# Kernel optimization log

Hardware: AMD Instinct MI355X
Metric: run time of the kernel (lower is better)

## Reference

```python
import jax, jax.numpy as jnp
import numpy as np

D_MODEL = 1024
H = 16
D_K = D_MODEL // H
MAX_SEQ_LEN = 2048
B = 2
S = 2048


def setup_inputs() -> dict:
    key = jax.random.key(0)
    ks = jax.random.split(key, 8)
    scale = 1.0 / np.sqrt(D_MODEL)
    return {
        "q": jax.random.normal(ks[0], (B, S, D_MODEL), jnp.float32),
        "k": jax.random.normal(ks[1], (B, S, D_MODEL), jnp.float32),
        "v": jax.random.normal(ks[2], (B, S, D_MODEL), jnp.float32),
        "mask": jnp.ones((B, 1, S, S), dtype=bool),
        "w_q": jax.random.normal(ks[3], (D_MODEL, D_MODEL), jnp.float32) * scale,
        "w_k": jax.random.normal(ks[4], (D_MODEL, D_MODEL), jnp.float32) * scale,
        "w_v": jax.random.normal(ks[5], (D_MODEL, D_MODEL), jnp.float32) * scale,
        "w_o": jax.random.normal(ks[6], (D_MODEL, D_MODEL), jnp.float32) * scale,
        "rel_emb": jax.random.normal(ks[7], (2 * MAX_SEQ_LEN - 1, H), jnp.float32) * 0.02,
    }


def reference(q, k, v, mask, w_q, w_k, w_v, w_o, rel_emb):
    batch, seq_len, _ = q.shape
    # projections (nn.Linear without bias: x @ W.T)
    query = (q @ w_q.T).reshape(batch, seq_len, H, D_K).transpose(0, 2, 1, 3)
    key_ = (k @ w_k.T).reshape(batch, seq_len, H, D_K).transpose(0, 2, 1, 3)
    value = (v @ w_v.T).reshape(batch, seq_len, H, D_K).transpose(0, 2, 1, 3)
    # scores: [B, H, S, S]
    scores = jnp.einsum("bhqd,bhkd->bhqk", query, key_) / jnp.sqrt(jnp.float32(D_K))
    # relative position bias
    rng = jnp.arange(seq_len)
    rel_pos = rng[:, None] - rng[None, :] + (MAX_SEQ_LEN - 1)  # [S, S]
    rel_bias = rel_emb[rel_pos]                                # [S, S, H]
    scores = scores + rel_bias.transpose(2, 0, 1)[None]        # [1, H, S, S]
    scores = jnp.where(mask, scores, -1e9)
    attn = jax.nn.softmax(scores, axis=-1)  # dropout p=0 -> identity
    x = jnp.einsum("bhqk,bhkd->bhqd", attn, value)
    x = x.transpose(0, 2, 1, 3).reshape(batch, seq_len, H * D_K)
    return x @ w_o.T
```

## Files before the change

kernel.cpp:

```cpp
#include <hip/hip_runtime.h>
#include <hip/hip_bf16.h>
#include <stdint.h>

typedef __bf16 bf16_t;
typedef __bf16 bf16x8 __attribute__((ext_vector_type(8)));
typedef __bf16 bf16x4 __attribute__((ext_vector_type(4)));
typedef float f32x4 __attribute__((ext_vector_type(4)));

#define D_MODEL 1024
#define NH 16
#define DK 64
#define SEQ 2048
#define BATCH 2
#define NKT (SEQ / 64)
#define LOG2E 1.44269504f

typedef const __attribute__((address_space(1))) void gas_void;
typedef __attribute__((address_space(3))) void las_void;
__device__ __forceinline__ void async16(const void* g, void* l) {
  __builtin_amdgcn_global_load_lds((gas_void*)g, (las_void*)l, 16, 0, 0);
}

__device__ __forceinline__ void bar_only() {
  asm volatile("s_barrier" ::: "memory");
}
__device__ __forceinline__ void bar_wait4() {
  asm volatile("s_waitcnt vmcnt(4)\n\ts_barrier" ::: "memory");
}
__device__ __forceinline__ void bar_wait0() {
  asm volatile("s_waitcnt vmcnt(0)\n\ts_barrier" ::: "memory");
}

__device__ __forceinline__ bf16x8 load8(const float* p) {
  float4 a = *(const float4*)p;
  float4 b = *(const float4*)(p + 4);
  bf16x8 r;
  r[0] = (bf16_t)a.x; r[1] = (bf16_t)a.y; r[2] = (bf16_t)a.z; r[3] = (bf16_t)a.w;
  r[4] = (bf16_t)b.x; r[5] = (bf16_t)b.y; r[6] = (bf16_t)b.z; r[7] = (bf16_t)b.w;
  return r;
}
__device__ __forceinline__ bf16x8 load8(const bf16_t* p) {
  return *(const bf16x8*)p;
}

__global__ __launch_bounds__(256) void cvt_all_kernel(
    const float* __restrict__ q, const float* __restrict__ k,
    const float* __restrict__ v,
    const float* __restrict__ wq, const float* __restrict__ wk,
    const float* __restrict__ wv, const float* __restrict__ wo,
    bf16_t* __restrict__ qb, bf16_t* __restrict__ kb, bf16_t* __restrict__ vb,
    bf16_t* __restrict__ wqb, bf16_t* __restrict__ wkb,
    bf16_t* __restrict__ wvb, bf16_t* __restrict__ wob)
{
  const int bx = blockIdx.x;
  const float* s; bf16_t* d; size_t base;
  if (bx < 6144) {
    int sel = bx >> 11;
    s = sel == 0 ? q : sel == 1 ? k : v;
    d = sel == 0 ? qb : sel == 1 ? kb : vb;
    base = (size_t)(bx & 2047) * 2048;
  } else {
    int sel = (bx - 6144) >> 9;
    s = sel == 0 ? wq : sel == 1 ? wk : sel == 2 ? wv : wo;
    d = sel == 0 ? wqb : sel == 1 ? wkb : sel == 2 ? wvb : wob;
    base = (size_t)((bx - 6144) & 511) * 2048;
  }
  size_t i = base + threadIdx.x * 8;
  *(bf16x8*)(d + i) = load8(s + i);
}

__device__ __forceinline__ void gemm_mainloop_async(
    const bf16_t* __restrict__ A, const bf16_t* __restrict__ W,
    int n0, int j0, bf16_t* As, bf16_t* Ws, f32x4 acc[4][4])
{
  const int tid  = threadIdx.x;
  const int wave = tid >> 6, lane = tid & 63;
  const int g = lane >> 4, rl = lane & 15;
  const int wm = (wave & 1) * 64, wn = (wave >> 1) * 64;

  for (int kt = 0; kt < D_MODEL / 64; ++kt) {
    __syncthreads();
#pragma unroll
    for (int i = 0; i < 4; ++i) {
      int c = tid + i * 256;
      int row = c >> 3, t = c & 7;
      int src = (t ^ (row & 7)) << 3;
      async16(A + (size_t)(n0 + row) * D_MODEL + kt * 64 + src, As + c * 8);
      async16(W + (size_t)(j0 + row) * D_MODEL + kt * 64 + src, Ws + c * 8);
    }
    __syncthreads();
#pragma unroll
    for (int kc = 0; kc < 2; ++kc) {
      bf16x8 af[4], bfr[4];
      const int j8 = ((kc * 4 + g) ^ (rl & 7)) << 3;
#pragma unroll
      for (int mi = 0; mi < 4; ++mi)
        af[mi] = *(const bf16x8*)(As + (wm + mi * 16 + rl) * 64 + j8);
#pragma unroll
      for (int ni = 0; ni < 4; ++ni)
        bfr[ni] = *(const bf16x8*)(Ws + (wn + ni * 16 + rl) * 64 + j8);
#pragma unroll
      for (int mi = 0; mi < 4; ++mi)
#pragma unroll
        for (int ni = 0; ni < 4; ++ni)
          acc[mi][ni] = __builtin_amdgcn_mfma_f32_16x16x32_bf16(
              af[mi], bfr[ni], acc[mi][ni], 0, 0, 0);
    }
  }
}

template <typename TA, typename TW>
__device__ __forceinline__ void gemm_mainloop_sync(const TA* __restrict__ A,
                                                   const TW* __restrict__ W,
                                                   int n0, int j0,
                                                   bf16_t* As, bf16_t* Ws,
                                                   f32x4 acc[4][4])
{
  const int tid  = threadIdx.x;
  const int wave = tid >> 6, lane = tid & 63;
  const int g = lane >> 4, rl = lane & 15;
  const int wm = (wave & 1) * 64, wn = (wave >> 1) * 64;

  for (int kt = 0; kt < D_MODEL / 64; ++kt) {
    __syncthreads();
#pragma unroll
    for (int i = 0; i < 4; ++i) {
      int c = tid + i * 256;
      int row = c >> 3, t = c & 7;
      *(bf16x8*)(As + row * 72 + t * 8) =
          load8(A + (size_t)(n0 + row) * D_MODEL + kt * 64 + t * 8);
      *(bf16x8*)(Ws + row * 72 + t * 8) =
          load8(W + (size_t)(j0 + row) * D_MODEL + kt * 64 + t * 8);
    }
    __syncthreads();
#pragma unroll
    for (int kc = 0; kc < 2; ++kc) {
      bf16x8 af[4], bfr[4];
#pragma unroll
      for (int mi = 0; mi < 4; ++mi)
        af[mi] = *(const bf16x8*)(As + (wm + mi * 16 + rl) * 72 + kc * 32 + g * 8);
#pragma unroll
      for (int ni = 0; ni < 4; ++ni)
        bfr[ni] = *(const bf16x8*)(Ws + (wn + ni * 16 + rl) * 72 + kc * 32 + g * 8);
#pragma unroll
      for (int mi = 0; mi < 4; ++mi)
#pragma unroll
        for (int ni = 0; ni < 4; ++ni)
          acc[mi][ni] = __builtin_amdgcn_mfma_f32_16x16x32_bf16(
              af[mi], bfr[ni], acc[mi][ni], 0, 0, 0);
    }
  }
}

__device__ __forceinline__ void qkv_epilogue(int which, int n0, int j0,
                                             f32x4 acc[4][4],
                                             bf16_t* qh, bf16_t* kh, bf16_t* vt)
{
  const int tid  = threadIdx.x;
  const int wave = tid >> 6, lane = tid & 63;
  const int g = lane >> 4, rl = lane & 15;
  const int wm = (wave & 1) * 64, wn = (wave >> 1) * 64;

  if (which == 2) {
    const int b = n0 >> 11;
#pragma unroll
    for (int mi = 0; mi < 4; ++mi)
#pragma unroll
      for (int ni = 0; ni < 4; ++ni) {
        bf16x4 pk;
#pragma unroll
        for (int r = 0; r < 4; ++r) pk[r] = (bf16_t)acc[mi][ni][r];
        int s = (n0 & (SEQ - 1)) + wm + mi * 16 + g * 4;
        int j = j0 + wn + ni * 16 + rl;
        int h = j >> 6, d = j & (DK - 1);
        int ktile = s >> 6, kloc = s & 63;
        *(bf16x4*)(vt + ((((size_t)(b * NH + h) * NKT + ktile) * DK + d) << 6) + kloc) = pk;
      }
  } else {
    bf16_t* O = (which == 0) ? qh : kh;
#pragma unroll
    for (int mi = 0; mi < 4; ++mi)
#pragma unroll
      for (int ni = 0; ni < 4; ++ni)
#pragma unroll
        for (int r = 0; r < 4; ++r) {
          int n = n0 + wm + mi * 16 + g * 4 + r;
          int j = j0 + wn + ni * 16 + rl;
          int b = n >> 11, s = n & (SEQ - 1);
          int h = j >> 6,  d = j & (DK - 1);
          O[((size_t)(b * NH + h) * SEQ + s) * DK + d] = (bf16_t)acc[mi][ni][r];
        }
  }
}

__global__ __launch_bounds__(256) void qkv_gemm_async(
    const bf16_t* __restrict__ qb, const bf16_t* __restrict__ kb,
    const bf16_t* __restrict__ vb,
    const bf16_t* __restrict__ wq, const bf16_t* __restrict__ wk,
    const bf16_t* __restrict__ wv,
    bf16_t* __restrict__ qh, bf16_t* __restrict__ kh, bf16_t* __restrict__ vt)
{
  __shared__ __align__(16) bf16_t smem[17408];
  bf16_t* As = smem;
  bf16_t* Ws = smem + 8192;

  const int jt = blockIdx.x, nt = blockIdx.y;
  const int which = jt >> 3;
  const int j0 = (jt & 7) * 128, n0 = nt * 128;
  const bf16_t* A = (which == 0) ? qb : (which == 1) ? kb : vb;
  const bf16_t* W = (which == 0) ? wq : (which == 1) ? wk : wv;
  f32x4 acc[4][4] = {};
  gemm_mainloop_async(A, W, n0, j0, As, Ws, acc);

  const int tid  = threadIdx.x;
  const int wave = tid >> 6, lane = tid & 63;
  const int g = lane >> 4, rl = lane & 15;
  const int wm = (wave & 1) * 64, wn = (wave >> 1) * 64;
  const int b = n0 >> 11, s0 = n0 & (SEQ - 1);

  if (which == 2) {
#pragma unroll
    for (int mi = 0; mi < 4; ++mi)
#pragma unroll
      for (int ni = 0; ni < 4; ++ni) {
        bf16x4 pk;
#pragma unroll
        for (int r = 0; r < 4; ++r) pk[r] = (bf16_t)acc[mi][ni][r];
        int s = s0 + wm + mi * 16 + g * 4;
        int j = j0 + wn + ni * 16 + rl;
        int h = j >> 6, d = j & (DK - 1);
        *(bf16x4*)(vt + ((((size_t)(b * NH + h) * NKT + (s >> 6)) * DK + d) << 6)
                   + (s & 63)) = pk;
      }
  } else {
    bf16_t* O = (which == 0) ? qh : kh;
    __syncthreads();
    bf16_t* T = smem;
#pragma unroll
    for (int mi = 0; mi < 4; ++mi)
#pragma unroll
      for (int ni = 0; ni < 4; ++ni)
#pragma unroll
        for (int r = 0; r < 4; ++r)
          T[(wm + mi * 16 + g * 4 + r) * 136 + wn + ni * 16 + rl] =
              (bf16_t)acc[mi][ni][r];
    __syncthreads();
#pragma unroll
    for (int i = 0; i < 8; ++i) {
      int cc = tid + i * 256;
      int row = cc >> 4, t = cc & 15;
      int j = j0 + t * 8;
      int h = j >> 6, d = j & (DK - 1);
      *(bf16x8*)(O + ((size_t)(b * NH + h) * SEQ + s0 + row) * DK + d) =
          *(const bf16x8*)(T + row * 136 + t * 8);
    }
  }
}

__global__ __launch_bounds__(256) void qkv_gemm_sync(
    const float* __restrict__ q, const float* __restrict__ k,
    const float* __restrict__ v,
    const float* __restrict__ wq, const float* __restrict__ wk,
    const float* __restrict__ wv,
    bf16_t* __restrict__ qh, bf16_t* __restrict__ kh, bf16_t* __restrict__ vt)
{
  __shared__ __align__(16) bf16_t As[128 * 72];
  __shared__ __align__(16) bf16_t Ws[128 * 72];
  const int jt = blockIdx.x, nt = blockIdx.y;
  const int which = jt >> 3;
  const int j0 = (jt & 7) * 128, n0 = nt * 128;
  const float* A = (which == 0) ? q : (which == 1) ? k : v;
  const float* W = (which == 0) ? wq : (which == 1) ? wk : wv;
  f32x4 acc[4][4] = {};
  gemm_mainloop_sync(A, W, n0, j0, As, Ws, acc);
  qkv_epilogue(which, n0, j0, acc, qh, kh, vt);
}

__device__ __forceinline__ void stage_kv(const bf16_t* Ktile, const bf16_t* Vtile,
                                         bf16_t* dK, bf16_t* dV, int tid)
{
#pragma unroll
  for (int i = 0; i < 2; ++i) {
    int c = tid + i * 256;
    int row = c >> 3, t = c & 7;
    int src = (t ^ (row & 7)) << 3;
    async16(Ktile + row * 64 + src, dK + c * 8);
    async16(Vtile + row * 64 + src, dV + c * 8);
  }
}

__global__ __launch_bounds__(256) void attn_kernel(
    const bf16_t* __restrict__ qh, const bf16_t* __restrict__ kh,
    const bf16_t* __restrict__ vt, const float* __restrict__ rel,
    bf16_t* __restrict__ xa)
{
  __shared__ __align__(16) bf16_t Ks[2][64 * 64];
  __shared__ __align__(16) bf16_t Vt[2][64 * 64];
  __shared__ __align__(16) bf16_t Ps[4][32 * 72];
  __shared__ float relw[2176];

  const int bx = blockIdx.x;
  const int qt = bx & 15;
  const int h  = (bx >> 4) & (NH - 1);
  const int b  = bx >> 8;
  const int q0 = qt * 128;

  const size_t headoff = (size_t)(b * NH + h) * SEQ * DK;
  const bf16_t* Q  = qh + headoff;
  const bf16_t* K  = kh + headoff;
  const bf16_t* Vg = vt + headoff;

  const int tid  = threadIdx.x;
  const int wave = tid >> 6, lane = tid & 63;
  const int g = lane >> 4, rl = lane & 15;
  const int rsw = rl & 7;

  for (int t = tid; t < 2175; t += 256)
    relw[t] = rel[(size_t)(q0 + t) * NH + h] * LOG2E;

  bf16x8 aq[2][2];
#pragma unroll
  for (int mb = 0; mb < 2; ++mb) {
    const int qrow = q0 + wave * 32 + mb * 16 + rl;
    aq[mb][0] = *(const bf16x8*)(Q + (size_t)qrow * DK + g * 8);
    aq[mb][1] = *(const bf16x8*)(Q + (size_t)qrow * DK + 32 + g * 8);
  }

  float lsum[2][4] = {};
  f32x4 o[2][4];
#pragma unroll
  for (int mb = 0; mb < 2; ++mb)
#pragma unroll
    for (int nb = 0; nb < 4; ++nb) o[mb][nb] = (f32x4){0.f, 0.f, 0.f, 0.f};

  __syncthreads();
  stage_kv(K, Vg, Ks[0], Vt[0], tid);

  for (int kt = 0; kt < NKT; ++kt) {
    const int p = kt & 1;
    const int k0 = kt * 64;
    const bf16_t* KsP = Ks[p];
    const bf16_t* VtP = Vt[p];

    bar_only();
    if (kt + 1 < NKT) {
      stage_kv(K + (size_t)(k0 + 64) * DK, Vg + (size_t)(kt + 1) * DK * 64,
               Ks[1 - p], Vt[1 - p], tid);
      bar_wait4();
    } else {
      bar_wait0();
    }

    bf16x8 kb0[4], kb1[4];
#pragma unroll
    for (int cb = 0; cb < 4; ++cb) {
      kb0[cb] = *(const bf16x8*)(KsP + (cb * 16 + rl) * 64 + ((g ^ rsw) << 3));
      kb1[cb] = *(const bf16x8*)(KsP + (cb * 16 + rl) * 64 + (((4 + g) ^ rsw) << 3));
    }

#pragma unroll
    for (int mb = 0; mb < 2; ++mb) {
#pragma unroll
      for (int cb = 0; cb < 4; ++cb) {
        f32x4 a = (f32x4){0.f, 0.f, 0.f, 0.f};
        a = __builtin_amdgcn_mfma_f32_16x16x32_bf16(aq[mb][0], kb0[cb], a, 0, 0, 0);
        a = __builtin_amdgcn_mfma_f32_16x16x32_bf16(aq[mb][1], kb1[cb], a, 0, 0, 0);
#pragma unroll
        for (int r = 0; r < 4; ++r) {
          const int iloc = wave * 32 + mb * 16 + g * 4 + r;
          const int jk = k0 + cb * 16 + rl;
          float pv = __builtin_amdgcn_exp2f(
              fmaf(a[r], 0.125f * LOG2E, relw[iloc - jk + 2047]));
          lsum[mb][r] += pv;
          Ps[wave][(mb * 16 + g * 4 + r) * 72 + cb * 16 + rl] = (bf16_t)pv;
        }
      }
    }
    __builtin_amdgcn_wave_barrier();

    bf16x8 vbf[2][4];
#pragma unroll
    for (int kc = 0; kc < 2; ++kc)
#pragma unroll
      for (int nb = 0; nb < 4; ++nb)
        vbf[kc][nb] = *(const bf16x8*)(VtP + (nb * 16 + rl) * 64 +
                                       (((kc * 4 + g) ^ rsw) << 3));

#pragma unroll
    for (int mb = 0; mb < 2; ++mb) {
#pragma unroll
      for (int kc = 0; kc < 2; ++kc) {
        bf16x8 ap = *(const bf16x8*)(&Ps[wave][(mb * 16 + rl) * 72 + kc * 32 + g * 8]);
#pragma unroll
        for (int nb = 0; nb < 4; ++nb)
          o[mb][nb] = __builtin_amdgcn_mfma_f32_16x16x32_bf16(ap, vbf[kc][nb],
                                                              o[mb][nb], 0, 0, 0);
      }
    }
    __builtin_amdgcn_wave_barrier();
  }

#pragma unroll
  for (int mask = 1; mask <= 8; mask <<= 1)
#pragma unroll
    for (int mb = 0; mb < 2; ++mb)
#pragma unroll
      for (int r = 0; r < 4; ++r)
        lsum[mb][r] += __shfl_xor(lsum[mb][r], mask, 64);

#pragma unroll
  for (int mb = 0; mb < 2; ++mb)
#pragma unroll
    for (int nb = 0; nb < 4; ++nb)
#pragma unroll
      for (int r = 0; r < 4; ++r) {
        const int srow = q0 + wave * 32 + mb * 16 + g * 4 + r;
        const int d = nb * 16 + rl;
        xa[(size_t)(b * SEQ + srow) * D_MODEL + h * DK + d] =
            (bf16_t)(o[mb][nb][r] / lsum[mb][r]);
      }
}

__global__ __launch_bounds__(256) void out_gemm_async(
    const bf16_t* __restrict__ xa, const bf16_t* __restrict__ wo,
    float* __restrict__ out)
{
  __shared__ __align__(16) bf16_t As[64 * 64];
  __shared__ __align__(16) bf16_t Ws[128 * 64];
  const int j0 = blockIdx.x * 128, n0 = blockIdx.y * 64;

  const int tid  = threadIdx.x;
  const int wave = tid >> 6, lane = tid & 63;
  const int g = lane >> 4, rl = lane & 15;
  const int wm = (wave & 1) * 32, wn = (wave >> 1) * 64;

  f32x4 acc[2][4] = {};
  for (int kt = 0; kt < D_MODEL / 64; ++kt) {
    __syncthreads();
#pragma unroll
    for (int i = 0; i < 2; ++i) {
      int c = tid + i * 256;
      int row = c >> 3, t = c & 7;
      int src = (t ^ (row & 7)) << 3;
      async16(xa + (size_t)(n0 + row) * D_MODEL + kt * 64 + src, As + c * 8);
    }
#pragma unroll
    for (int i = 0; i < 4; ++i) {
      int c = tid + i * 256;
      int row = c >> 3, t = c & 7;
      int src = (t ^ (row & 7)) << 3;
      async16(wo + (size_t)(j0 + row) * D_MODEL + kt * 64 + src, Ws + c * 8);
    }
    __syncthreads();
#pragma unroll
    for (int kc = 0; kc < 2; ++kc) {
      bf16x8 af[2], bfr[4];
      const int j8 = ((kc * 4 + g) ^ (rl & 7)) << 3;
#pragma unroll
      for (int mi = 0; mi < 2; ++mi)
        af[mi] = *(const bf16x8*)(As + (wm + mi * 16 + rl) * 64 + j8);
#pragma unroll
      for (int ni = 0; ni < 4; ++ni)
        bfr[ni] = *(const bf16x8*)(Ws + (wn + ni * 16 + rl) * 64 + j8);
#pragma unroll
      for (int mi = 0; mi < 2; ++mi)
#pragma unroll
        for (int ni = 0; ni < 4; ++ni)
          acc[mi][ni] = __builtin_amdgcn_mfma_f32_16x16x32_bf16(
              af[mi], bfr[ni], acc[mi][ni], 0, 0, 0);
    }
  }

#pragma unroll
  for (int mi = 0; mi < 2; ++mi)
#pragma unroll
    for (int ni = 0; ni < 4; ++ni)
#pragma unroll
      for (int r = 0; r < 4; ++r) {
        int n = n0 + wm + mi * 16 + g * 4 + r;
        int j = j0 + wn + ni * 16 + rl;
        out[(size_t)n * D_MODEL + j] = acc[mi][ni][r];
      }
}

__global__ __launch_bounds__(256) void out_gemm_sync(
    const bf16_t* __restrict__ xa, const float* __restrict__ wo,
    float* __restrict__ out)
{
  __shared__ __align__(16) bf16_t As[128 * 72];
  __shared__ __align__(16) bf16_t Ws[128 * 72];
  const int j0 = blockIdx.x * 128, n0 = blockIdx.y * 128;
  f32x4 acc[4][4] = {};
  gemm_mainloop_sync(xa, wo, n0, j0, As, Ws, acc);

  const int tid  = threadIdx.x;
  const int wave = tid >> 6, lane = tid & 63;
  const int g = lane >> 4, rl = lane & 15;
  const int wm = (wave & 1) * 64, wn = (wave >> 1) * 64;
#pragma unroll
  for (int mi = 0; mi < 4; ++mi)
#pragma unroll
    for (int ni = 0; ni < 4; ++ni)
#pragma unroll
      for (int r = 0; r < 4; ++r) {
        int n = n0 + wm + mi * 16 + g * 4 + r;
        int j = j0 + wn + ni * 16 + rl;
        out[(size_t)n * D_MODEL + j] = acc[mi][ni][r];
      }
}

extern "C" void kernel_launch(void* const* d_in, const int* in_sizes, int n_in,
                              void* d_out, int out_size, void* d_ws, size_t ws_size,
                              hipStream_t stream)
{
  const float* q   = (const float*)d_in[0];
  const float* k   = (const float*)d_in[1];
  const float* v   = (const float*)d_in[2];
  const float* wq  = (const float*)d_in[4];
  const float* wk  = (const float*)d_in[5];
  const float* wv  = (const float*)d_in[6];
  const float* wo  = (const float*)d_in[7];
  const float* rel = (const float*)d_in[8];
  float* out = (float*)d_out;

  char* ws = (char*)d_ws;
  const size_t seg  = (size_t)BATCH * SEQ * D_MODEL * sizeof(bf16_t);
  const size_t wseg = (size_t)D_MODEL * D_MODEL * sizeof(bf16_t);
  const size_t need = 6 * seg + 4 * wseg;

  if (ws_size >= need) {
    bf16_t* qb  = (bf16_t*)(ws);
    bf16_t* kb  = (bf16_t*)(ws + seg);
    bf16_t* vb  = (bf16_t*)(ws + 2 * seg);
    bf16_t* wqb = (bf16_t*)(ws + 3 * seg);
    bf16_t* wkb = (bf16_t*)(ws + 3 * seg + wseg);
    bf16_t* wvb = (bf16_t*)(ws + 3 * seg + 2 * wseg);
    bf16_t* wob = (bf16_t*)(ws + 3 * seg + 3 * wseg);
    bf16_t* qh  = (bf16_t*)(ws + 3 * seg + 4 * wseg);
    bf16_t* kh  = (bf16_t*)(ws + 4 * seg + 4 * wseg);
    bf16_t* vt  = (bf16_t*)(ws + 5 * seg + 4 * wseg);
    bf16_t* xa  = qb;

    cvt_all_kernel<<<dim3(8192), 256, 0, stream>>>(q, k, v, wq, wk, wv, wo,
                                                   qb, kb, vb, wqb, wkb, wvb, wob);
    qkv_gemm_async<<<dim3(24, 32), 256, 0, stream>>>(qb, kb, vb, wqb, wkb, wvb,
                                                     qh, kh, vt);
    attn_kernel<<<dim3(512), 256, 0, stream>>>(qh, kh, vt, rel, xa);
    out_gemm_async<<<dim3(8, 64), 256, 0, stream>>>(xa, wob, out);
  } else {
    bf16_t* qh = (bf16_t*)(ws);
    bf16_t* kh = (bf16_t*)(ws + seg);
    bf16_t* vt = (bf16_t*)(ws + 2 * seg);
    bf16_t* xa = (bf16_t*)(ws + 3 * seg);
    qkv_gemm_sync<<<dim3(24, 32), 256, 0, stream>>>(q, k, v, wq, wk, wv,
                                                    qh, kh, vt);
    attn_kernel<<<dim3(512), 256, 0, stream>>>(qh, kh, vt, rel, xa);
    out_gemm_sync<<<dim3(8, 32), 256, 0, stream>>>(xa, wo, out);
  }
}
```

Before: 268.4 us.

## Fuse activation conversion into QKV GEMM and keep attention P in registers

Drops the separate fp32-to-bf16 conversion of q/k/v: the QKV GEMM now loads fp32 activations and converts while staging to LDS, and only the weights are pre-converted. The attention kernel computes S transposed so the probability fragments stay in registers and feed 16x16x16 MFMAs directly, which removes the per-wave P round trip through LDS. The same rewrite also drops the double-buffered K/V prefetch for single-buffered loads with two block barriers per tile. Activation staging becomes synchronous instead of async global-to-LDS, and the lost K/V overlap may expose memory latency.

```diff
diff --git a/kernel.cpp b/kernel.cpp
--- a/kernel.cpp
+++ b/kernel.cpp
@@ -5,7 +5,8 @@
 typedef __bf16 bf16_t;
 typedef __bf16 bf16x8 __attribute__((ext_vector_type(8)));
 typedef __bf16 bf16x4 __attribute__((ext_vector_type(4)));
-typedef float f32x4 __attribute__((ext_vector_type(4)));
+typedef short  s16x4  __attribute__((ext_vector_type(4)));
+typedef float  f32x4  __attribute__((ext_vector_type(4)));
 
 #define D_MODEL 1024
 #define NH 16
@@ -21,16 +22,6 @@
   __builtin_amdgcn_global_load_lds((gas_void*)g, (las_void*)l, 16, 0, 0);
 }
 
-__device__ __forceinline__ void bar_only() {
-  asm volatile("s_barrier" ::: "memory");
-}
-__device__ __forceinline__ void bar_wait4() {
-  asm volatile("s_waitcnt vmcnt(4)\n\ts_barrier" ::: "memory");
-}
-__device__ __forceinline__ void bar_wait0() {
-  asm volatile("s_waitcnt vmcnt(0)\n\ts_barrier" ::: "memory");
-}
-
 __device__ __forceinline__ bf16x8 load8(const float* p) {
   float4 a = *(const float4*)p;
   float4 b = *(const float4*)(p + 4);
@@ -43,34 +34,43 @@
   return *(const bf16x8*)p;
 }
 
-__global__ __launch_bounds__(256) void cvt_all_kernel(
-    const float* __restrict__ q, const float* __restrict__ k,
-    const float* __restrict__ v,
-    const float* __restrict__ wq, const float* __restrict__ wk,
-    const float* __restrict__ wv, const float* __restrict__ wo,
-    bf16_t* __restrict__ qb, bf16_t* __restrict__ kb, bf16_t* __restrict__ vb,
-    bf16_t* __restrict__ wqb, bf16_t* __restrict__ wkb,
-    bf16_t* __restrict__ wvb, bf16_t* __restrict__ wob)
-{
-  const int bx = blockIdx.x;
-  const float* s; bf16_t* d; size_t base;
-  if (bx < 6144) {
-    int sel = bx >> 11;
-    s = sel == 0 ? q : sel == 1 ? k : v;
-    d = sel == 0 ? qb : sel == 1 ? kb : vb;
-    base = (size_t)(bx & 2047) * 2048;
-  } else {
-    int sel = (bx - 6144) >> 9;
-    s = sel == 0 ? wq : sel == 1 ? wk : sel == 2 ? wv : wo;
-    d = sel == 0 ? wqb : sel == 1 ? wkb : sel == 2 ? wvb : wob;
-    base = (size_t)((bx - 6144) & 511) * 2048;
-  }
-  size_t i = base + threadIdx.x * 8;
+__device__ __forceinline__ f32x4 mfma16x16x16_bf16(bf16x4 a, bf16x4 b, f32x4 c) {
+#if __has_builtin(__builtin_amdgcn_mfma_f32_16x16x16_bf16)
+  return __builtin_amdgcn_mfma_f32_16x16x16_bf16(a, b, c, 0, 0, 0);
+#else
+  union { bf16x4 h; s16x4 s; } ua, ub;
+  ua.h = a; ub.h = b;
+  return __builtin_amdgcn_mfma_f32_16x16x16bf16_1k(ua.s, ub.s, c, 0, 0, 0);
+#endif
+}
+
+__global__ __launch_bounds__(256) void wcvt_kernel(
+    const float* __restrict__ w0, const float* __restrict__ w1,
+    const float* __restrict__ w2, const float* __restrict__ w3,
+    bf16_t* __restrict__ o0, bf16_t* __restrict__ o1,
+    bf16_t* __restrict__ o2, bf16_t* __restrict__ o3)
+{
+  const float* s; bf16_t* d;
+  switch (blockIdx.y) {
+    case 0:  s = w0; d = o0; break;
+    case 1:  s = w1; d = o1; break;
+    case 2:  s = w2; d = o2; break;
+    default: s = w3; d = o3; break;
+  }
+  size_t i = (size_t)(blockIdx.x * 256 + threadIdx.x) * 8;
   *(bf16x8*)(d + i) = load8(s + i);
 }
 
+__device__ __forceinline__ void stage_chunk(const bf16_t* g, bf16_t* l) {
+  async16(g, l);
+}
+__device__ __forceinline__ void stage_chunk(const float* g, bf16_t* l) {
+  *(bf16x8*)l = load8(g);
+}
+
+template <typename TA>
 __device__ __forceinline__ void gemm_mainloop_async(
-    const bf16_t* __restrict__ A, const bf16_t* __restrict__ W,
+    const TA* __restrict__ A, const bf16_t* __restrict__ W,
     int n0, int j0, bf16_t* As, bf16_t* Ws, f32x4 acc[4][4])
 {
   const int tid  = threadIdx.x;
@@ -85,7 +85,7 @@
       int c = tid + i * 256;
       int row = c >> 3, t = c & 7;
       int src = (t ^ (row & 7)) << 3;
-      async16(A + (size_t)(n0 + row) * D_MODEL + kt * 64 + src, As + c * 8);
+      stage_chunk(A + (size_t)(n0 + row) * D_MODEL + kt * 64 + src, As + c * 8);
       async16(W + (size_t)(j0 + row) * D_MODEL + kt * 64 + src, Ws + c * 8);
     }
     __syncthreads();
@@ -173,8 +173,8 @@
         int s = (n0 & (SEQ - 1)) + wm + mi * 16 + g * 4;
         int j = j0 + wn + ni * 16 + rl;
         int h = j >> 6, d = j & (DK - 1);
-        int ktile = s >> 6, kloc = s & 63;
-        *(bf16x4*)(vt + ((((size_t)(b * NH + h) * NKT + ktile) * DK + d) << 6) + kloc) = pk;
+        *(bf16x4*)(vt + ((((size_t)(b * NH + h) * NKT + (s >> 6)) * DK + d) << 6)
+                   + (s & 63)) = pk;
       }
   } else {
     bf16_t* O = (which == 0) ? qh : kh;
@@ -194,8 +194,8 @@
 }
 
 __global__ __launch_bounds__(256) void qkv_gemm_async(
-    const bf16_t* __restrict__ qb, const bf16_t* __restrict__ kb,
-    const bf16_t* __restrict__ vb,
+    const float* __restrict__ q, const float* __restrict__ k,
+    const float* __restrict__ v,
     const bf16_t* __restrict__ wq, const bf16_t* __restrict__ wk,
     const bf16_t* __restrict__ wv,
     bf16_t* __restrict__ qh, bf16_t* __restrict__ kh, bf16_t* __restrict__ vt)
@@ -207,7 +207,7 @@
   const int jt = blockIdx.x, nt = blockIdx.y;
   const int which = jt >> 3;
   const int j0 = (jt & 7) * 128, n0 = nt * 128;
-  const bf16_t* A = (which == 0) ? qb : (which == 1) ? kb : vb;
+  const float*  A = (which == 0) ? q : (which == 1) ? k : v;
   const bf16_t* W = (which == 0) ? wq : (which == 1) ? wk : wv;
   f32x4 acc[4][4] = {};
   gemm_mainloop_async(A, W, n0, j0, As, Ws, acc);
@@ -219,19 +219,7 @@
   const int b = n0 >> 11, s0 = n0 & (SEQ - 1);
 
   if (which == 2) {
-#pragma unroll
-    for (int mi = 0; mi < 4; ++mi)
-#pragma unroll
-      for (int ni = 0; ni < 4; ++ni) {
-        bf16x4 pk;
-#pragma unroll
-        for (int r = 0; r < 4; ++r) pk[r] = (bf16_t)acc[mi][ni][r];
-        int s = s0 + wm + mi * 16 + g * 4;
-        int j = j0 + wn + ni * 16 + rl;
-        int h = j >> 6, d = j & (DK - 1);
-        *(bf16x4*)(vt + ((((size_t)(b * NH + h) * NKT + (s >> 6)) * DK + d) << 6)
-                   + (s & 63)) = pk;
-      }
+    qkv_epilogue(2, n0, j0, acc, qh, kh, vt);
   } else {
     bf16_t* O = (which == 0) ? qh : kh;
     __syncthreads();
@@ -276,27 +264,13 @@
   qkv_epilogue(which, n0, j0, acc, qh, kh, vt);
 }
 
-__device__ __forceinline__ void stage_kv(const bf16_t* Ktile, const bf16_t* Vtile,
-                                         bf16_t* dK, bf16_t* dV, int tid)
-{
-#pragma unroll
-  for (int i = 0; i < 2; ++i) {
-    int c = tid + i * 256;
-    int row = c >> 3, t = c & 7;
-    int src = (t ^ (row & 7)) << 3;
-    async16(Ktile + row * 64 + src, dK + c * 8);
-    async16(Vtile + row * 64 + src, dV + c * 8);
-  }
-}
-
 __global__ __launch_bounds__(256) void attn_kernel(
     const bf16_t* __restrict__ qh, const bf16_t* __restrict__ kh,
     const bf16_t* __restrict__ vt, const float* __restrict__ rel,
     bf16_t* __restrict__ xa)
 {
-  __shared__ __align__(16) bf16_t Ks[2][64 * 64];
-  __shared__ __align__(16) bf16_t Vt[2][64 * 64];
-  __shared__ __align__(16) bf16_t Ps[4][32 * 72];
+  __shared__ __align__(16) bf16_t Ks[64 * 64];
+  __shared__ __align__(16) bf16_t Vt[64 * 64];
   __shared__ float relw[2176];
 
   const int bx = blockIdx.x;
@@ -326,87 +300,89 @@
     aq[mb][1] = *(const bf16x8*)(Q + (size_t)qrow * DK + 32 + g * 8);
   }
 
-  float lsum[2][4] = {};
+  float lsum[2] = {0.f, 0.f};
   f32x4 o[2][4];
 #pragma unroll
   for (int mb = 0; mb < 2; ++mb)
 #pragma unroll
     for (int nb = 0; nb < 4; ++nb) o[mb][nb] = (f32x4){0.f, 0.f, 0.f, 0.f};
 
-  __syncthreads();
-  stage_kv(K, Vg, Ks[0], Vt[0], tid);
-
   for (int kt = 0; kt < NKT; ++kt) {
-    const int p = kt & 1;
     const int k0 = kt * 64;
-    const bf16_t* KsP = Ks[p];
-    const bf16_t* VtP = Vt[p];
-
-    bar_only();
-    if (kt + 1 < NKT) {
-      stage_kv(K + (size_t)(k0 + 64) * DK, Vg + (size_t)(kt + 1) * DK * 64,
-               Ks[1 - p], Vt[1 - p], tid);
-      bar_wait4();
-    } else {
-      bar_wait0();
-    }
+    const bf16_t* Ktile = K + (size_t)k0 * DK;
+    const bf16_t* Vtile = Vg + (size_t)kt * DK * 64;
+    __syncthreads();
+#pragma unroll
+    for (int i = 0; i < 2; ++i) {
+      int c = tid + i * 256;
+      int row = c >> 3, t = c & 7;
+      int src = (t ^ (row & 7)) << 3;
+      async16(Ktile + row * 64 + src, Ks + c * 8);
+      async16(Vtile + row * 64 + src, Vt + c * 8);
+    }
+    __syncthreads();
 
     bf16x8 kb0[4], kb1[4];
 #pragma unroll
     for (int cb = 0; cb < 4; ++cb) {
-      kb0[cb] = *(const bf16x8*)(KsP + (cb * 16 + rl) * 64 + ((g ^ rsw) << 3));
-      kb1[cb] = *(const bf16x8*)(KsP + (cb * 16 + rl) * 64 + (((4 + g) ^ rsw) << 3));
-    }
-
+      kb0[cb] = *(const bf16x8*)(Ks + (cb * 16 + rl) * 64 + ((g ^ rsw) << 3));
+      kb1[cb] = *(const bf16x8*)(Ks + (cb * 16 + rl) * 64 + (((4 + g) ^ rsw) << 3));
+    }
+    bf16x4 vf[4][4];
+#pragma unroll
+    for (int nb = 0; nb < 4; ++nb)
+#pragma unroll
+      for (int cb = 0; cb < 4; ++cb)
+        vf[nb][cb] = *(const bf16x4*)(Vt + (nb * 16 + rl) * 64 +
+                                      (((2 * cb + (g >> 1)) ^ rsw) << 3) +
+                                      4 * (g & 1));
+
+    bf16x4 pf[2][4];
 #pragma unroll
     for (int mb = 0; mb < 2; ++mb) {
+      const int iloc = wave * 32 + mb * 16 + rl;
 #pragma unroll
       for (int cb = 0; cb < 4; ++cb) {
         f32x4 a = (f32x4){0.f, 0.f, 0.f, 0.f};
-        a = __builtin_amdgcn_mfma_f32_16x16x32_bf16(aq[mb][0], kb0[cb], a, 0, 0, 0);
-        a = __builtin_amdgcn_mfma_f32_16x16x32_bf16(aq[mb][1], kb1[cb], a, 0, 0, 0);
+        a = __builtin_amdgcn_mfma_f32_16x16x32_bf16(kb0[cb], aq[mb][0], a, 0, 0, 0);
+        a = __builtin_amdgcn_mfma_f32_16x16x32_bf16(kb1[cb], aq[mb][1], a, 0, 0, 0);
+        const int base = iloc - (k0 + cb * 16 + g * 4) + 2047;
+        float ls = 0.f;
+        bf16x4 pk;
 #pragma unroll
         for (int r = 0; r < 4; ++r) {
-          const int iloc = wave * 32 + mb * 16 + g * 4 + r;
-          const int jk = k0 + cb * 16 + rl;
           float pv = __builtin_amdgcn_exp2f(
-              fmaf(a[r], 0.125f * LOG2E, relw[iloc - jk + 2047]));
-          lsum[mb][r] += pv;
-          Ps[wave][(mb * 16 + g * 4 + r) * 72 + cb * 16 + rl] = (bf16_t)pv;
+              fmaf(a[r], 0.125f * LOG2E, relw[base - r]));
+          ls += pv;
+          pk[r] = (bf16_t)pv;
         }
+        lsum[mb] += ls;
+        pf[mb][cb] = pk;
       }
     }
-    __builtin_amdgcn_wave_barrier();
-
-    bf16x8 vbf[2][4];
-#pragma unroll
-    for (int kc = 0; kc < 2; ++kc)
+
+#pragma unroll
+    for (int mb = 0; mb < 2; ++mb)
 #pragma unroll
       for (int nb = 0; nb < 4; ++nb)
-        vbf[kc][nb] = *(const bf16x8*)(VtP + (nb * 16 + rl) * 64 +
-                                       (((kc * 4 + g) ^ rsw) << 3));
-
-#pragma unroll
-    for (int mb = 0; mb < 2; ++mb) {
-#pragma unroll
-      for (int kc = 0; kc < 2; ++kc) {
-        bf16x8 ap = *(const bf16x8*)(&Ps[wave][(mb * 16 + rl) * 72 + kc * 32 + g * 8]);
-#pragma unroll
-        for (int nb = 0; nb < 4; ++nb)
-          o[mb][nb] = __builtin_amdgcn_mfma_f32_16x16x32_bf16(ap, vbf[kc][nb],
-                                                              o[mb][nb], 0, 0, 0);
-      }
-    }
-    __builtin_amdgcn_wave_barrier();
-  }
-
-#pragma unroll
-  for (int mask = 1; mask <= 8; mask <<= 1)
-#pragma unroll
-    for (int mb = 0; mb < 2; ++mb)
-#pragma unroll
-      for (int r = 0; r < 4; ++r)
-        lsum[mb][r] += __shfl_xor(lsum[mb][r], mask, 64);
+#pragma unroll
+        for (int cb = 0; cb < 4; ++cb)
+          o[mb][nb] = mfma16x16x16_bf16(pf[mb][cb], vf[nb][cb], o[mb][nb]);
+  }
+
+  float rinv[2];
+#pragma unroll
+  for (int mb = 0; mb < 2; ++mb) {
+    lsum[mb] += __shfl_xor(lsum[mb], 16, 64);
+    lsum[mb] += __shfl_xor(lsum[mb], 32, 64);
+    rinv[mb] = 1.f / lsum[mb];
+  }
+  float w[2][4];
+#pragma unroll
+  for (int mb = 0; mb < 2; ++mb)
+#pragma unroll
+    for (int r = 0; r < 4; ++r)
+      w[mb][r] = __shfl(rinv[mb], g * 4 + r, 64);
 
 #pragma unroll
   for (int mb = 0; mb < 2; ++mb)
@@ -417,7 +393,7 @@
         const int srow = q0 + wave * 32 + mb * 16 + g * 4 + r;
         const int d = nb * 16 + rl;
         xa[(size_t)(b * SEQ + srow) * D_MODEL + h * DK + d] =
-            (bf16_t)(o[mb][nb][r] / lsum[mb][r]);
+            (bf16_t)(o[mb][nb][r] * w[mb][r]);
       }
 }
 
@@ -526,24 +502,21 @@
   char* ws = (char*)d_ws;
   const size_t seg  = (size_t)BATCH * SEQ * D_MODEL * sizeof(bf16_t);
   const size_t wseg = (size_t)D_MODEL * D_MODEL * sizeof(bf16_t);
-  const size_t need = 6 * seg + 4 * wseg;
+  const size_t need = 4 * seg + 4 * wseg;
 
   if (ws_size >= need) {
-    bf16_t* qb  = (bf16_t*)(ws);
-    bf16_t* kb  = (bf16_t*)(ws + seg);
-    bf16_t* vb  = (bf16_t*)(ws + 2 * seg);
-    bf16_t* wqb = (bf16_t*)(ws + 3 * seg);
-    bf16_t* wkb = (bf16_t*)(ws + 3 * seg + wseg);
-    bf16_t* wvb = (bf16_t*)(ws + 3 * seg + 2 * wseg);
-    bf16_t* wob = (bf16_t*)(ws + 3 * seg + 3 * wseg);
-    bf16_t* qh  = (bf16_t*)(ws + 3 * seg + 4 * wseg);
-    bf16_t* kh  = (bf16_t*)(ws + 4 * seg + 4 * wseg);
-    bf16_t* vt  = (bf16_t*)(ws + 5 * seg + 4 * wseg);
-    bf16_t* xa  = qb;
-
-    cvt_all_kernel<<<dim3(8192), 256, 0, stream>>>(q, k, v, wq, wk, wv, wo,
-                                                   qb, kb, vb, wqb, wkb, wvb, wob);
-    qkv_gemm_async<<<dim3(24, 32), 256, 0, stream>>>(qb, kb, vb, wqb, wkb, wvb,
+    bf16_t* wqb = (bf16_t*)(ws);
+    bf16_t* wkb = (bf16_t*)(ws + wseg);
+    bf16_t* wvb = (bf16_t*)(ws + 2 * wseg);
+    bf16_t* wob = (bf16_t*)(ws + 3 * wseg);
+    bf16_t* qh  = (bf16_t*)(ws + 4 * wseg);
+    bf16_t* kh  = (bf16_t*)(ws + 4 * wseg + seg);
+    bf16_t* vt  = (bf16_t*)(ws + 4 * wseg + 2 * seg);
+    bf16_t* xa  = (bf16_t*)(ws + 4 * wseg + 3 * seg);
+
+    wcvt_kernel<<<dim3(512, 4), 256, 0, stream>>>(wq, wk, wv, wo,
+                                                  wqb, wkb, wvb, wob);
+    qkv_gemm_async<<<dim3(24, 32), 256, 0, stream>>>(q, k, v, wqb, wkb, wvb,
                                                      qh, kh, vt);
     attn_kernel<<<dim3(512), 256, 0, stream>>>(qh, kh, vt, rel, xa);
     out_gemm_async<<<dim3(8, 64), 256, 0, stream>>>(xa, wob, out);
```

New measurement: 273.9 us. 2.1% more time.
